# Optimization experiments

Measured on AMD Instinct MI355X. Metric: run time of the kernel, lower is better.

The kernel has to match this reference:

```python
import jax, jax.numpy as jnp
import numpy as np

N_HEADS = 12


def setup_inputs() -> dict:
    key = jax.random.key(0)
    k1, k2, k3 = jax.random.split(key, 3)
    B, W, C = 2, 2048, 768
    in_sequence_bwc = jax.random.normal(k1, (B, W, C), dtype=jnp.float32)
    # QKV projection weight [3C, C] (torch Linear convention: out_features x in_features)
    w_attn = jax.random.normal(k2, (3 * C, C), dtype=jnp.float32) * (1.0 / np.sqrt(C))
    w_proj = jax.random.normal(k3, (C, C), dtype=jnp.float32) * (1.0 / np.sqrt(C))
    return {"in_sequence_bwc": in_sequence_bwc, "w_attn": w_attn, "w_proj": w_proj}


def reference(in_sequence_bwc, w_attn, w_proj):
    B, W, C = in_sequence_bwc.shape
    H = N_HEADS
    K = C // H  # head dim
    qkv = jnp.einsum('bwc,dc->bwd', in_sequence_bwc, w_attn)  # [B,W,3C]
    q, k, v = jnp.split(qkv, 3, axis=-1)
    # [B,H,W,K]
    q = q.reshape(B, W, H, K).transpose(0, 2, 1, 3)
    k = k.reshape(B, W, H, K).transpose(0, 2, 1, 3)
    v = v.reshape(B, W, H, K).transpose(0, 2, 1, 3)
    scores = jnp.einsum('bhqk,bhsk->bhqs', q, k) / jnp.sqrt(jnp.float32(K))
    causal = jnp.tril(jnp.ones((W, W), dtype=bool))
    scores = jnp.where(causal[None, None], scores, jnp.float32(-jnp.inf))
    probs = jax.nn.softmax(scores, axis=-1)
    out = jnp.einsum('bhqs,bhsk->bhqk', probs, v)  # [B,H,W,K]
    out = out.transpose(0, 2, 1, 3).reshape(B, W, C)
    return jnp.einsum('bwc,dc->bwd', out, w_proj)
```

## Files before the change

kernel.cpp:

```cpp
#include <hip/hip_runtime.h>

constexpr int B_  = 2;
constexpr int W_  = 2048;
constexpr int C_  = 768;
constexpr int H_  = 12;
constexpr int HD  = 64;
constexpr int C3  = 3 * C_;
constexpr int M_  = B_ * W_;
constexpr int NSLOT = 80;

typedef float  f32x4 __attribute__((ext_vector_type(4)));
typedef short  s16x8 __attribute__((ext_vector_type(8)));
typedef short  s16x4 __attribute__((ext_vector_type(4)));
typedef unsigned short u16;
typedef unsigned int   u32;

__device__ __forceinline__ u16 f2bf(float f) {
    unsigned int u = __float_as_uint(f);
    u += 0x7FFFu + ((u >> 16) & 1u);
    return (u16)(u >> 16);
}

__device__ __forceinline__ void gload_lds16(const u16* g, u16* l) {
    __builtin_amdgcn_global_load_lds(
        (const __attribute__((address_space(1))) unsigned int*)g,
        (__attribute__((address_space(3))) unsigned int*)l, 16, 0, 0);
}

__global__ __launch_bounds__(256)
void cvt_all(const float* __restrict__ x, const float* __restrict__ wa,
             const float* __restrict__ wp, u16* __restrict__ xb,
             u16* __restrict__ wab, u16* __restrict__ wpb)
{
    const int n0 = M_ * C_ / 8;
    const int n1 = n0 + C3 * C_ / 8;
    const int n2 = n1 + C_ * C_ / 8;
    int i = blockIdx.x * 256 + threadIdx.x;
    const float* s; u16* d; int j;
    if (i < n0)      { s = x;  d = xb;  j = i; }
    else if (i < n1) { s = wa; d = wab; j = i - n0; }
    else if (i < n2) { s = wp; d = wpb; j = i - n1; }
    else return;
    const float4 a = reinterpret_cast<const float4*>(s)[j * 2];
    const float4 b = reinterpret_cast<const float4*>(s)[j * 2 + 1];
    s16x8 v;
    v[0] = (short)f2bf(a.x); v[1] = (short)f2bf(a.y);
    v[2] = (short)f2bf(a.z); v[3] = (short)f2bf(a.w);
    v[4] = (short)f2bf(b.x); v[5] = (short)f2bf(b.y);
    v[6] = (short)f2bf(b.z); v[7] = (short)f2bf(b.w);
    reinterpret_cast<s16x8*>(d)[j] = v;
}

__device__ __forceinline__ void store_out(u16*  p, float v) { *p = f2bf(v); }
__device__ __forceinline__ void store_out(float* p, float v) { *p = v; }

template <typename OutT>
__global__ __launch_bounds__(256)
void gemm_nt_mfma(const u16* __restrict__ A, const u16* __restrict__ Bm,
                  OutT* __restrict__ Y, int Ndim, int Kdim)
{
    __shared__ __align__(16) u16 As[2][128 * 64];
    __shared__ __align__(16) u16 Bs[2][128 * 64];

    const int t  = threadIdx.x;
    const int w  = t >> 6;
    const int l  = t & 63;
    const int lg = l >> 4;
    const int ln = l & 15;
    const int wm = w >> 1;
    const int wn = w & 1;
    const int m0 = blockIdx.x * 128;
    const int n0 = blockIdx.y * 128;

    f32x4 acc[4][4];
    #pragma unroll
    for (int mi = 0; mi < 4; ++mi)
        #pragma unroll
        for (int ni = 0; ni < 4; ++ni)
            acc[mi][ni] = (f32x4){0.f, 0.f, 0.f, 0.f};

    #define GEMM_STAGE(buf, k0s)                                              \
        _Pragma("unroll")                                                     \
        for (int it = 0; it < 4; ++it) {                                      \
            const int c  = t + it * 256;                                      \
            const int fr = c >> 7;                                            \
            const int s  = (c >> 6) & 1;                                      \
            const int kc = (c >> 4) & 3;                                      \
            const int rr = c & 15;                                            \
            const size_t koff = (size_t)(k0s) + s * 32 + kc * 8;              \
            gload_lds16(A  + (size_t)(m0 + fr * 16 + rr) * Kdim + koff,       \
                        &As[buf][(size_t)(it * 256 + w * 64) * 8]);           \
            gload_lds16(Bm + (size_t)(n0 + fr * 16 + rr) * Kdim + koff,       \
                        &Bs[buf][(size_t)(it * 256 + w * 64) * 8]);           \
        }

    GEMM_STAGE(0, 0)
    __syncthreads();

    int cur = 0;
    for (int k0 = 0; k0 < Kdim; k0 += 64) {
        if (k0 + 64 < Kdim) { GEMM_STAGE(cur ^ 1, k0 + 64) }

        #pragma unroll
        for (int s = 0; s < 2; ++s) {
            s16x8 af[4], bf[4];
            #pragma unroll
            for (int mi = 0; mi < 4; ++mi)
                af[mi] = *reinterpret_cast<const s16x8*>(
                    &As[cur][(size_t)((wm * 4 + mi) * 128 + s * 64 + lg * 16 + ln) * 8]);
            #pragma unroll
            for (int ni = 0; ni < 4; ++ni)
                bf[ni] = *reinterpret_cast<const s16x8*>(
                    &Bs[cur][(size_t)((wn * 4 + ni) * 128 + s * 64 + lg * 16 + ln) * 8]);
            __builtin_amdgcn_s_setprio(1);
            #pragma unroll
            for (int mi = 0; mi < 4; ++mi)
                #pragma unroll
                for (int ni = 0; ni < 4; ++ni)
                    acc[mi][ni] = __builtin_amdgcn_mfma_f32_16x16x32_bf16(
                        af[mi], bf[ni], acc[mi][ni], 0, 0, 0);
            __builtin_amdgcn_s_setprio(0);
        }

        __syncthreads();
        cur ^= 1;
    }
    #undef GEMM_STAGE

    #pragma unroll
    for (int mi = 0; mi < 4; ++mi) {
        const int row = m0 + wm * 64 + mi * 16 + lg * 4;
        #pragma unroll
        for (int ni = 0; ni < 4; ++ni) {
            const int col = n0 + wn * 64 + ni * 16 + ln;
            #pragma unroll
            for (int r = 0; r < 4; ++r)
                store_out(&Y[(size_t)(row + r) * Ndim + col], acc[mi][ni][r]);
        }
    }
}

__global__ __launch_bounds__(256)
void attn_partial(const u16* __restrict__ qkv, float* __restrict__ po,
                  float* __restrict__ pl)
{
    __shared__ __align__(16) unsigned char KsB[64 * 128];
    __shared__ __align__(16) unsigned char VtB[64 * 144];

    const int t  = threadIdx.x;
    const int w  = t >> 6;
    const int l  = t & 63;
    const int lg = l >> 4;
    const int ln = l & 15;
    const int p  = blockIdx.x;
    const int h  = blockIdx.y;
    const int b  = blockIdx.z;

    int qt, ck;
    if (p < 8)       { qt = p;                 ck = 0; }
    else if (p < 24) { qt = 8  + ((p - 8) >> 1);  ck = (p - 8) & 1; }
    else if (p < 48) { qt = 16 + (p - 24) / 3;    ck = (p - 24) % 3; }
    else             { qt = 24 + ((p - 48) >> 2); ck = (p - 48) & 3; }

    const int qb  = qt * 64;
    const int q0w = qb + w * 16;
    const int g0  = ck * 8;
    const int g1  = min(qt + 1, g0 + 8);
    const int slot = (b * H_ + h) * NSLOT + p;

    const u16* base  = qkv + (size_t)(b * W_) * C3;
    const u16* kbase = base + C_ + h * HD;
    const u16* vbase = base + 2 * C_ + h * HD;

    s16x8 qf[2];
    {
        const u16* qrow = base + (size_t)(q0w + ln) * C3 + h * HD;
        #pragma unroll
        for (int kc = 0; kc < 2; ++kc)
            qf[kc] = *reinterpret_cast<const s16x8*>(&qrow[kc * 32 + lg * 8]);
    }

    s16x8 onesf;
    {
        const short v1 = (ln == 0) ? (short)0x3F80 : (short)0;
        #pragma unroll
        for (int i = 0; i < 8; ++i) onesf[i] = v1;
    }

    f32x4 o[4];
    #pragma unroll
    for (int i = 0; i < 4; ++i) o[i] = (f32x4){0.f, 0.f, 0.f, 0.f};
    f32x4 o4 = (f32x4){0.f, 0.f, 0.f, 0.f};

    const float c1 = 0.18033688011112042f;
    const float c2 = 17.312340490667562f;

    const size_t sk_off = (size_t)((t >> 7) * 16 + (t & 15)) * C3
                        + ((t >> 6) & 1) * 32 + ((t >> 4) & 3) * 8;
    const bool vstage = (t < 128);
    const int vrun = (t >> 4) & 7;
    const int vK0  = (vrun >> 2) * 32 + (vrun & 3) * 4;
    const int vdq  = (t & 15) * 4;
    const int kfb  = l * 16;

    s16x8 kr[2];
    s16x4 vr[8];

    {
        const int s0 = g0 * 64;
        const u16* ks = kbase + (size_t)s0 * C3 + sk_off;
        kr[0] = *reinterpret_cast<const s16x8*>(ks);
        kr[1] = *reinterpret_cast<const s16x8*>(ks + (size_t)32 * C3);
        if (vstage) {
            const u16* vsrc = vbase + (size_t)(s0 + vK0) * C3 + vdq;
            #pragma unroll
            for (int e = 0; e < 8; ++e)
                vr[e] = *reinterpret_cast<const s16x4*>(
                    &vsrc[(size_t)((e >> 2) * 16 + (e & 3)) * C3]);
        }
    }

    for (int g = g0; g < g1; ++g) {
        const int s0 = g * 64;

        __syncthreads();

        *reinterpret_cast<s16x8*>(KsB + t * 16)         = kr[0];
        *reinterpret_cast<s16x8*>(KsB + (t + 256) * 16) = kr[1];
        if (vstage) {
            #pragma unroll
            for (int j = 0; j < 4; ++j) {
                s16x8 pk = { vr[0][j], vr[1][j], vr[2][j], vr[3][j],
                             vr[4][j], vr[5][j], vr[6][j], vr[7][j] };
                *reinterpret_cast<s16x8*>(
                    VtB + (vdq + j) * 144 + vrun * 16) = pk;
            }
        }

        if (g + 1 < g1) {
            const int s1 = s0 + 64;
            const u16* ks = kbase + (size_t)s1 * C3 + sk_off;
            kr[0] = *reinterpret_cast<const s16x8*>(ks);
            kr[1] = *reinterpret_cast<const s16x8*>(ks + (size_t)32 * C3);
            if (vstage) {
                const u16* vsrc = vbase + (size_t)(s1 + vK0) * C3 + vdq;
                #pragma unroll
                for (int e = 0; e < 8; ++e)
                    vr[e] = *reinterpret_cast<const s16x4*>(
                        &vsrc[(size_t)((e >> 2) * 16 + (e & 3)) * C3]);
            }
        }

        __syncthreads();

        #pragma unroll
        for (int c = 0; c < 2; ++c) {
            if (s0 + c * 32 <= q0w + 15) {
                float pt[2][4];
                #pragma unroll
                for (int n2 = 0; n2 < 2; ++n2) {
                    const unsigned char* kfrag = KsB + (c * 2 + n2) * 2048 + kfb;
                    s16x8 kf0 = *reinterpret_cast<const s16x8*>(kfrag);
                    s16x8 kf1 = *reinterpret_cast<const s16x8*>(kfrag + 1024);
                    f32x4 s = (f32x4){0.f, 0.f, 0.f, 0.f};
                    __builtin_amdgcn_s_setprio(1);
                    s = __builtin_amdgcn_mfma_f32_16x16x32_bf16(kf0, qf[0], s, 0, 0, 0);
                    s = __builtin_amdgcn_mfma_f32_16x16x32_bf16(kf1, qf[1], s, 0, 0, 0);
                    __builtin_amdgcn_s_setprio(0);
                    const int kg0   = s0 + c * 32 + n2 * 16 + lg * 4;
                    const int klast = s0 + c * 32 + n2 * 16 + 15;
                    if (klast <= q0w) {
                        #pragma unroll
                        for (int r = 0; r < 4; ++r)
                            pt[n2][r] = exp2f(fmaf(s[r], c1, -c2));
                    } else {
                        const int qg = q0w + ln;
                        #pragma unroll
                        for (int r = 0; r < 4; ++r)
                            pt[n2][r] = (kg0 + r <= qg)
                                      ? exp2f(fmaf(s[r], c1, -c2)) : 0.0f;
                    }
                }
                union { s16x8 v; u32 wd[4]; } afu;
                asm("v_cvt_pk_bf16_f32 %0, %1, %2"
                    : "=v"(afu.wd[0]) : "v"(pt[0][0]), "v"(pt[0][1]));
                asm("v_cvt_pk_bf16_f32 %0, %1, %2"
                    : "=v"(afu.wd[1]) : "v"(pt[0][2]), "v"(pt[0][3]));
                asm("v_cvt_pk_bf16_f32 %0, %1, %2"
                    : "=v"(afu.wd[2]) : "v"(pt[1][0]), "v"(pt[1][1]));
                asm("v_cvt_pk_bf16_f32 %0, %1, %2"
                    : "=v"(afu.wd[3]) : "v"(pt[1][2]), "v"(pt[1][3]));
                const s16x8 af = afu.v;
                s16x8 vf[4];
                #pragma unroll
                for (int dt = 0; dt < 4; ++dt)
                    vf[dt] = *reinterpret_cast<const s16x8*>(
                        VtB + (dt * 16 + ln) * 144 + c * 64 + lg * 16);
                __builtin_amdgcn_s_setprio(1);
                #pragma unroll
                for (int dt = 0; dt < 4; ++dt)
                    o[dt] = __builtin_amdgcn_mfma_f32_16x16x32_bf16(af, vf[dt], o[dt], 0, 0, 0);
                o4 = __builtin_amdgcn_mfma_f32_16x16x32_bf16(af, onesf, o4, 0, 0, 0);
                __builtin_amdgcn_s_setprio(0);
            }
        }
    }

    if (ln == 0) {
        #pragma unroll
        for (int r = 0; r < 4; ++r)
            pl[(size_t)slot * 64 + w * 16 + lg * 4 + r] = o4[r];
    }
    float* os = po + (size_t)slot * 4096;
    #pragma unroll
    for (int r = 0; r < 4; ++r)
        #pragma unroll
        for (int dt = 0; dt < 4; ++dt)
            os[(w * 16 + lg * 4 + r) * 64 + dt * 16 + ln] = o[dt][r];
}

__global__ __launch_bounds__(256)
void attn_combine(const float* __restrict__ po, const float* __restrict__ pl,
                  u16* __restrict__ aob)
{
    const int qt = blockIdx.x;
    const int h  = blockIdx.y;
    const int b  = blockIdx.z;
    const int nc = (qt + 8) >> 3;
    int cum;
    if (qt < 8)       cum = qt;
    else if (qt < 16) cum = 8  + 2 * (qt - 8);
    else if (qt < 24) cum = 24 + 3 * (qt - 16);
    else              cum = 48 + 4 * (qt - 24);
    const int slot0 = (b * H_ + h) * NSLOT + cum;

    const int tid = threadIdx.x;
    const int i   = tid >> 2;
    const int d0  = (tid & 3) * 16;

    f32x4 acc[4] = { (f32x4){0,0,0,0}, (f32x4){0,0,0,0},
                     (f32x4){0,0,0,0}, (f32x4){0,0,0,0} };
    float lt = 0.0f;
    for (int c = 0; c < nc; ++c) {
        const float* os = po + (size_t)(slot0 + c) * 4096 + i * 64 + d0;
        #pragma unroll
        for (int v = 0; v < 4; ++v)
            acc[v] += *reinterpret_cast<const f32x4*>(os + v * 4);
        lt += pl[(size_t)(slot0 + c) * 64 + i];
    }
    const float inv = 1.0f / lt;

    u16* dst = aob + (size_t)(b * W_ + qt * 64 + i) * C_ + h * HD + d0;
    s16x8 ov[2];
    #pragma unroll
    for (int v = 0; v < 4; ++v)
        #pragma unroll
        for (int e = 0; e < 4; ++e)
            ov[v >> 1][(v & 1) * 4 + e] = (short)f2bf(acc[v][e] * inv);
    *reinterpret_cast<s16x8*>(dst)     = ov[0];
    *reinterpret_cast<s16x8*>(dst + 8) = ov[1];
}

extern "C" void kernel_launch(void* const* d_in, const int* in_sizes, int n_in,
                              void* d_out, int out_size, void* d_ws, size_t ws_size,
                              hipStream_t stream)
{
    const float* x      = (const float*)d_in[0];
    const float* w_attn = (const float*)d_in[1];
    const float* w_proj = (const float*)d_in[2];
    float* out = (float*)d_out;

    u16* xb   = (u16*)d_ws;
    u16* wab  = xb   + (size_t)M_ * C_;
    u16* wpb  = wab  + (size_t)C3 * C_;
    u16* qkvb = wpb  + (size_t)C_ * C_;
    u16* aob  = qkvb + (size_t)M_ * C3;
    float* po = (float*)(aob + (size_t)M_ * C_);
    float* pl = po + (size_t)B_ * H_ * NSLOT * 4096;

    {
        const int total8 = (M_ * C_ + C3 * C_ + C_ * C_) / 8;
        cvt_all<<<(total8 + 255) / 256, 256, 0, stream>>>(
            x, w_attn, w_proj, xb, wab, wpb);
    }

    {
        dim3 grid(M_ / 128, C3 / 128);
        gemm_nt_mfma<u16><<<grid, 256, 0, stream>>>(xb, wab, qkvb, C3, C_);
    }

    {
        dim3 grid(NSLOT, H_, B_);
        attn_partial<<<grid, 256, 0, stream>>>(qkvb, po, pl);
    }
    {
        dim3 grid(W_ / 64, H_, B_);
        attn_combine<<<grid, 256, 0, stream>>>(po, pl, aob);
    }

    {
        dim3 grid(M_ / 128, C_ / 128);
        gemm_nt_mfma<float><<<grid, 256, 0, stream>>>(aob, wpb, out, C_, C_);
    }
}
```

Before: 126.2 us.

## Fuse activation fp32-to-bf16 conversion into QKV GEMM and store partials as bf16

```diff
diff --git a/kernel.cpp b/kernel.cpp
--- a/kernel.cpp
+++ b/kernel.cpp
@@ -20,6 +20,9 @@
     u += 0x7FFFu + ((u >> 16) & 1u);
     return (u16)(u >> 16);
 }
+__device__ __forceinline__ float bf2f(u16 v) {
+    return __uint_as_float(((u32)v) << 16);
+}
 
 __device__ __forceinline__ void gload_lds16(const u16* g, u16* l) {
     __builtin_amdgcn_global_load_lds(
@@ -28,18 +31,15 @@
 }
 
 __global__ __launch_bounds__(256)
-void cvt_all(const float* __restrict__ x, const float* __restrict__ wa,
-             const float* __restrict__ wp, u16* __restrict__ xb,
-             u16* __restrict__ wab, u16* __restrict__ wpb)
+void cvt_w(const float* __restrict__ wa, const float* __restrict__ wp,
+           u16* __restrict__ wab, u16* __restrict__ wpb)
 {
-    const int n0 = M_ * C_ / 8;
-    const int n1 = n0 + C3 * C_ / 8;
-    const int n2 = n1 + C_ * C_ / 8;
+    const int n0 = C3 * C_ / 8;
+    const int n1 = n0 + C_ * C_ / 8;
     int i = blockIdx.x * 256 + threadIdx.x;
     const float* s; u16* d; int j;
-    if (i < n0)      { s = x;  d = xb;  j = i; }
-    else if (i < n1) { s = wa; d = wab; j = i - n0; }
-    else if (i < n2) { s = wp; d = wpb; j = i - n1; }
+    if (i < n0)      { s = wa; d = wab; j = i; }
+    else if (i < n1) { s = wp; d = wpb; j = i - n0; }
     else return;
     const float4 a = reinterpret_cast<const float4*>(s)[j * 2];
     const float4 b = reinterpret_cast<const float4*>(s)[j * 2 + 1];
@@ -54,11 +54,12 @@
 __device__ __forceinline__ void store_out(u16*  p, float v) { *p = f2bf(v); }
 __device__ __forceinline__ void store_out(float* p, float v) { *p = v; }
 
-template <typename OutT>
+template <typename AT, typename OutT>
 __global__ __launch_bounds__(256)
-void gemm_nt_mfma(const u16* __restrict__ A, const u16* __restrict__ Bm,
+void gemm_nt_mfma(const AT* __restrict__ A, const u16* __restrict__ Bm,
                   OutT* __restrict__ Y, int Ndim, int Kdim)
 {
+    constexpr bool A32 = (sizeof(AT) == 4);
     __shared__ __align__(16) u16 As[2][128 * 64];
     __shared__ __align__(16) u16 Bs[2][128 * 64];
 
@@ -79,35 +80,89 @@
         for (int ni = 0; ni < 4; ++ni)
             acc[mi][ni] = (f32x4){0.f, 0.f, 0.f, 0.f};
 
-    #define GEMM_STAGE(buf, k0s)                                              \
-        _Pragma("unroll")                                                     \
-        for (int it = 0; it < 4; ++it) {                                      \
-            const int c  = t + it * 256;                                      \
-            const int fr = c >> 7;                                            \
-            const int s  = (c >> 6) & 1;                                      \
-            const int kc = (c >> 4) & 3;                                      \
-            const int rr = c & 15;                                            \
-            const size_t koff = (size_t)(k0s) + s * 32 + kc * 8;              \
-            gload_lds16(A  + (size_t)(m0 + fr * 16 + rr) * Kdim + koff,       \
-                        &As[buf][(size_t)(it * 256 + w * 64) * 8]);           \
-            gload_lds16(Bm + (size_t)(n0 + fr * 16 + rr) * Kdim + koff,       \
-                        &Bs[buf][(size_t)(it * 256 + w * 64) * 8]);           \
-        }
-
-    GEMM_STAGE(0, 0)
-    __syncthreads();
+    size_t off[4];
+    #pragma unroll
+    for (int it = 0; it < 4; ++it) {
+        const int c  = t + it * 256;
+        off[it] = (size_t)((c >> 7) * 16 + (c & 15)) * Kdim
+                + ((c >> 6) & 1) * 32 + ((c >> 4) & 3) * 8;
+    }
+
+    f32x4 ar[8];
+
+    if constexpr (A32) {
+        #pragma unroll
+        for (int it = 0; it < 4; ++it) {
+            const float* ga = A + (size_t)m0 * Kdim + off[it];
+            ar[2 * it]     = *reinterpret_cast<const f32x4*>(ga);
+            ar[2 * it + 1] = *reinterpret_cast<const f32x4*>(ga + 4);
+        }
+    } else {
+        #pragma unroll
+        for (int it = 0; it < 4; ++it)
+            gload_lds16((const u16*)A + (size_t)m0 * Kdim + off[it],
+                        &As[0][(size_t)(it * 256 + w * 64) * 8]);
+    }
+    #pragma unroll
+    for (int it = 0; it < 4; ++it)
+        gload_lds16(Bm + (size_t)n0 * Kdim + off[it],
+                    &Bs[0][(size_t)(it * 256 + w * 64) * 8]);
 
     int cur = 0;
     for (int k0 = 0; k0 < Kdim; k0 += 64) {
-        if (k0 + 64 < Kdim) { GEMM_STAGE(cur ^ 1, k0 + 64) }
-
+        __syncthreads();
+
+        if constexpr (A32) {
+            #pragma unroll
+            for (int it = 0; it < 4; ++it) {
+                union { s16x8 v; u32 wd[4]; } pk;
+                asm("v_cvt_pk_bf16_f32 %0, %1, %2"
+                    : "=v"(pk.wd[0]) : "v"(ar[2*it][0]), "v"(ar[2*it][1]));
+                asm("v_cvt_pk_bf16_f32 %0, %1, %2"
+                    : "=v"(pk.wd[1]) : "v"(ar[2*it][2]), "v"(ar[2*it][3]));
+                asm("v_cvt_pk_bf16_f32 %0, %1, %2"
+                    : "=v"(pk.wd[2]) : "v"(ar[2*it+1][0]), "v"(ar[2*it+1][1]));
+                asm("v_cvt_pk_bf16_f32 %0, %1, %2"
+                    : "=v"(pk.wd[3]) : "v"(ar[2*it+1][2]), "v"(ar[2*it+1][3]));
+                *reinterpret_cast<s16x8*>(&As[0][(size_t)(t + it * 256) * 8]) = pk.v;
+            }
+        }
+
+        if (k0 + 64 < Kdim) {
+            if constexpr (A32) {
+                #pragma unroll
+                for (int it = 0; it < 4; ++it) {
+                    const float* ga = A + (size_t)m0 * Kdim + k0 + 64 + off[it];
+                    ar[2 * it]     = *reinterpret_cast<const f32x4*>(ga);
+                    ar[2 * it + 1] = *reinterpret_cast<const f32x4*>(ga + 4);
+                }
+            } else {
+                #pragma unroll
+                for (int it = 0; it < 4; ++it)
+                    gload_lds16((const u16*)A + (size_t)m0 * Kdim + k0 + 64 + off[it],
+                                &As[cur ^ 1][(size_t)(it * 256 + w * 64) * 8]);
+            }
+            #pragma unroll
+            for (int it = 0; it < 4; ++it)
+                gload_lds16(Bm + (size_t)n0 * Kdim + k0 + 64 + off[it],
+                            &Bs[cur ^ 1][(size_t)(it * 256 + w * 64) * 8]);
+        }
+
+        if constexpr (A32) {
+            asm volatile("s_waitcnt lgkmcnt(0)" ::: "memory");
+            __builtin_amdgcn_sched_barrier(0);
+            __builtin_amdgcn_s_barrier();
+            __builtin_amdgcn_sched_barrier(0);
+        }
+
+        const u16* Asr = A32 ? As[0] : As[cur];
         #pragma unroll
         for (int s = 0; s < 2; ++s) {
             s16x8 af[4], bf[4];
             #pragma unroll
             for (int mi = 0; mi < 4; ++mi)
                 af[mi] = *reinterpret_cast<const s16x8*>(
-                    &As[cur][(size_t)((wm * 4 + mi) * 128 + s * 64 + lg * 16 + ln) * 8]);
+                    &Asr[(size_t)((wm * 4 + mi) * 128 + s * 64 + lg * 16 + ln) * 8]);
             #pragma unroll
             for (int ni = 0; ni < 4; ++ni)
                 bf[ni] = *reinterpret_cast<const s16x8*>(
@@ -121,11 +176,8 @@
                         af[mi], bf[ni], acc[mi][ni], 0, 0, 0);
             __builtin_amdgcn_s_setprio(0);
         }
-
-        __syncthreads();
         cur ^= 1;
     }
-    #undef GEMM_STAGE
 
     #pragma unroll
     for (int mi = 0; mi < 4; ++mi) {
@@ -141,7 +193,7 @@
 }
 
 __global__ __launch_bounds__(256)
-void attn_partial(const u16* __restrict__ qkv, float* __restrict__ po,
+void attn_partial(const u16* __restrict__ qkv, u16* __restrict__ po,
                   float* __restrict__ pl)
 {
     __shared__ __align__(16) unsigned char KsB[64 * 128];
@@ -311,16 +363,16 @@
         for (int r = 0; r < 4; ++r)
             pl[(size_t)slot * 64 + w * 16 + lg * 4 + r] = o4[r];
     }
-    float* os = po + (size_t)slot * 4096;
+    u16* os = po + (size_t)slot * 4096;
     #pragma unroll
     for (int r = 0; r < 4; ++r)
         #pragma unroll
         for (int dt = 0; dt < 4; ++dt)
-            os[(w * 16 + lg * 4 + r) * 64 + dt * 16 + ln] = o[dt][r];
+            os[(w * 16 + lg * 4 + r) * 64 + dt * 16 + ln] = f2bf(o[dt][r]);
 }
 
 __global__ __launch_bounds__(256)
-void attn_combine(const float* __restrict__ po, const float* __restrict__ pl,
+void attn_combine(const u16* __restrict__ po, const float* __restrict__ pl,
                   u16* __restrict__ aob)
 {
     const int qt = blockIdx.x;
@@ -338,14 +390,17 @@
     const int i   = tid >> 2;
     const int d0  = (tid & 3) * 16;
 
-    f32x4 acc[4] = { (f32x4){0,0,0,0}, (f32x4){0,0,0,0},
-                     (f32x4){0,0,0,0}, (f32x4){0,0,0,0} };
+    float acc[16] = {};
     float lt = 0.0f;
     for (int c = 0; c < nc; ++c) {
-        const float* os = po + (size_t)(slot0 + c) * 4096 + i * 64 + d0;
-        #pragma unroll
-        for (int v = 0; v < 4; ++v)
-            acc[v] += *reinterpret_cast<const f32x4*>(os + v * 4);
+        const u16* os = po + (size_t)(slot0 + c) * 4096 + i * 64 + d0;
+        s16x8 v0 = *reinterpret_cast<const s16x8*>(os);
+        s16x8 v1 = *reinterpret_cast<const s16x8*>(os + 8);
+        #pragma unroll
+        for (int e = 0; e < 8; ++e) {
+            acc[e]     += bf2f((u16)v0[e]);
+            acc[8 + e] += bf2f((u16)v1[e]);
+        }
         lt += pl[(size_t)(slot0 + c) * 64 + i];
     }
     const float inv = 1.0f / lt;
@@ -353,10 +408,10 @@
     u16* dst = aob + (size_t)(b * W_ + qt * 64 + i) * C_ + h * HD + d0;
     s16x8 ov[2];
     #pragma unroll
-    for (int v = 0; v < 4; ++v)
-        #pragma unroll
-        for (int e = 0; e < 4; ++e)
-            ov[v >> 1][(v & 1) * 4 + e] = (short)f2bf(acc[v][e] * inv);
+    for (int e = 0; e < 8; ++e) {
+        ov[0][e] = (short)f2bf(acc[e] * inv);
+        ov[1][e] = (short)f2bf(acc[8 + e] * inv);
+    }
     *reinterpret_cast<s16x8*>(dst)     = ov[0];
     *reinterpret_cast<s16x8*>(dst + 8) = ov[1];
 }
@@ -370,23 +425,21 @@
     const float* w_proj = (const float*)d_in[2];
     float* out = (float*)d_out;
 
-    u16* xb   = (u16*)d_ws;
-    u16* wab  = xb   + (size_t)M_ * C_;
+    u16* wab  = (u16*)d_ws;
     u16* wpb  = wab  + (size_t)C3 * C_;
     u16* qkvb = wpb  + (size_t)C_ * C_;
     u16* aob  = qkvb + (size_t)M_ * C3;
-    float* po = (float*)(aob + (size_t)M_ * C_);
-    float* pl = po + (size_t)B_ * H_ * NSLOT * 4096;
-
-    {
-        const int total8 = (M_ * C_ + C3 * C_ + C_ * C_) / 8;
-        cvt_all<<<(total8 + 255) / 256, 256, 0, stream>>>(
-            x, w_attn, w_proj, xb, wab, wpb);
+    u16* po   = aob  + (size_t)M_ * C_;
+    float* pl = (float*)(po + (size_t)B_ * H_ * NSLOT * 4096);
+
+    {
+        const int total8 = (C3 * C_ + C_ * C_) / 8;
+        cvt_w<<<(total8 + 255) / 256, 256, 0, stream>>>(w_attn, w_proj, wab, wpb);
     }
 
     {
         dim3 grid(M_ / 128, C3 / 128);
-        gemm_nt_mfma<u16><<<grid, 256, 0, stream>>>(xb, wab, qkvb, C3, C_);
+        gemm_nt_mfma<float, u16><<<grid, 256, 0, stream>>>(x, wab, qkvb, C3, C_);
     }
 
     {
@@ -400,6 +453,6 @@
 
     {
         dim3 grid(M_ / 128, C_ / 128);
-        gemm_nt_mfma<float><<<grid, 256, 0, stream>>>(aob, wpb, out, C_, C_);
-    }
-}
+        gemm_nt_mfma<u16, float><<<grid, 256, 0, stream>>>(aob, wpb, out, C_, C_);
+    }
+}
```

Measured after the change: 137.5 us. 1.09x slower.
